# Optimization experiments

Measured on AMD Instinct MI355X. Metric: run time of the kernel, lower is better.

Reference implementation:

```python
import jax, jax.numpy as jnp
import numpy as np

B, S, H, T = 64, 512, 768, 50


def setup_inputs() -> dict:
    key = jax.random.key(0)
    k1, k2, k3, k4, k5, k6, k7 = jax.random.split(key, 7)
    full_hidden = jax.random.normal(k1, (B, S, H), dtype=jnp.float32)
    tag_ids = jax.random.randint(k2, (B, S), 0, T)
    lengths = jax.random.randint(k3, (B,), 1, S + 1)
    mask = (jnp.arange(S)[None, :] < lengths[:, None])  # valid-prefix mask, t=0 always on
    W = jax.random.normal(k4, (H, T), dtype=jnp.float32) * 0.02
    b = jnp.zeros((T,), dtype=jnp.float32)
    start_transitions = jax.random.normal(k5, (T,), dtype=jnp.float32) * 0.1
    end_transitions = jax.random.normal(k6, (T,), dtype=jnp.float32) * 0.1
    transitions = jax.random.normal(k7, (T, T), dtype=jnp.float32) * 0.1
    return {
        'full_hidden': full_hidden, 'W': W, 'b': b,
        'start_transitions': start_transitions, 'end_transitions': end_transitions,
        'transitions': transitions, 'tag_ids': tag_ids, 'mask': mask,
    }


def _crf_losses(emissions, start_transitions, end_transitions, transitions, tag_ids, mask):
    # emissions: [B,S,T]; returns per-sequence loss = log_partition - gold_score (pytorch-crf, reduction='none', negated)
    maskf = mask.astype(emissions.dtype)
    Bn = tag_ids.shape[0]
    bidx = jnp.arange(Bn)
    # ---- numerator: score of the gold tag path ----
    em_tag = jnp.take_along_axis(emissions, tag_ids[..., None], axis=2)[..., 0]  # [B,S]
    num = start_transitions[tag_ids[:, 0]] + em_tag[:, 0]
    trans_score = transitions[tag_ids[:, :-1], tag_ids[:, 1:]]  # [B,S-1]
    num = num + jnp.sum((trans_score + em_tag[:, 1:]) * maskf[:, 1:], axis=1)
    lengths = jnp.sum(mask.astype(jnp.int32), axis=1)
    last_tags = tag_ids[bidx, lengths - 1]
    num = num + end_transitions[last_tags]
    # ---- denominator: log partition via forward DP (scan over time) ----
    alpha0 = start_transitions[None, :] + emissions[:, 0]  # [B,T]

    def step(alpha, inp):
        em_t, m_t = inp  # [B,T], [B]
        nxt = jax.nn.logsumexp(alpha[:, :, None] + transitions[None, :, :] + em_t[:, None, :], axis=1)
        alpha = jnp.where(m_t[:, None], nxt, alpha)
        return alpha, None

    em_rest = jnp.swapaxes(emissions[:, 1:], 0, 1)  # [S-1,B,T]
    m_rest = jnp.swapaxes(mask[:, 1:], 0, 1)        # [S-1,B]
    alpha, _ = jax.lax.scan(step, alpha0, (em_rest, m_rest))
    den = jax.nn.logsumexp(alpha + end_transitions[None, :], axis=1)
    return den - num  # [B]


def reference(full_hidden, W, b, start_transitions, end_transitions, transitions, tag_ids, mask):
    # dropout is identity in eval mode (config dropout applied at train time only)
    emissions = jnp.einsum('bsh,ht->bst', full_hidden, W) + b  # hid2tag
    return _crf_losses(emissions, start_transitions, end_transitions, transitions, tag_ids, mask)
```

## Files before the change

kernel.cpp:

```cpp
#include <hip/hip_runtime.h>
#include <cstdint>
#include <cstddef>

#define Bn 64
#define Sn 512
#define Hn 768
#define Tn 50
#define CH 32
#define NCH 16
#define EP 52

typedef short short8 __attribute__((ext_vector_type(8)));
typedef float floatx4 __attribute__((ext_vector_type(4)));

__device__ __forceinline__ uint32_t rne_bf16(float x) {
  uint32_t u = __float_as_uint(x);
  return (u + 0x7FFFu + ((u >> 16) & 1u)) >> 16;
}
__device__ __forceinline__ uint32_t pack2(float a, float b) {
  return rne_bf16(a) | (rne_bf16(b) << 16);
}
__device__ __forceinline__ float rdlane(float v, int i) {
  return __uint_as_float(__builtin_amdgcn_readlane(__float_as_uint(v), i));
}

__global__ __launch_bounds__(256) void prep_kernel(
    const float* __restrict__ W, const float* __restrict__ trans,
    const int* __restrict__ mask, uint32_t* __restrict__ wfrag,
    int* __restrict__ lenbuf, float* __restrict__ Ee,
    float* __restrict__ EeT) {
  const int blk = blockIdx.x;
  const int tid = threadIdx.x;
  if (blk < 64) {
    if (tid < 64) {
      int s = 0;
      for (int t = tid; t < Sn; t += 64) s += mask[blk * Sn + t];
#pragma unroll
      for (int off = 1; off < 64; off <<= 1) s += __shfl_xor(s, off);
      if (tid == 0) lenbuf[blk] = s;
    }
    return;
  }
  if (blk == 88) {
    for (int gid = tid; gid < Tn * Tn; gid += 256) {
      const int r = gid / Tn, cl = gid - r * Tn;
      const float v = __expf(trans[gid]);
      Ee[r * EP + cl] = v;
      EeT[cl * EP + r] = v;
    }
    return;
  }
  const int gid = (blk - 64) * 256 + tid;
  const int f = gid >> 6;
  const int l = gid & 63;
  const int ks = f >> 2, nt = f & 3;
  const int col = nt * 16 + (l & 15);
  const int k0 = ks * 32 + (l >> 4) * 8;
  float v[8];
#pragma unroll
  for (int j = 0; j < 8; ++j)
    v[j] = (col < Tn) ? W[(size_t)(k0 + j) * Tn + col] : 0.f;
  uint4 d;
  d.x = pack2(v[0], v[1]);
  d.y = pack2(v[2], v[3]);
  d.z = pack2(v[4], v[5]);
  d.w = pack2(v[6], v[7]);
  ((uint4*)wfrag)[gid] = d;
}

#define BK 64
__global__ __launch_bounds__(256, 1) void emissions_kernel(
    const float* __restrict__ hidden, const uint32_t* __restrict__ wfrag,
    const float* __restrict__ bias, const int* __restrict__ lenbuf,
    float* __restrict__ em) {
  const int blk = blockIdx.x;
  const int bb = blk >> 3, cc = blk & 7;
  if (cc * 64 >= lenbuf[bb]) return;
  const int tid = threadIdx.x;
  const int lane = tid & 63;
  const int w = tid >> 6;
  const int g = lane >> 4;
  const int li = lane & 15;
  const int row0 = blk * 64;
  __shared__ char lds_raw[64 * 128];

  floatx4 acc[4];
#pragma unroll
  for (int nt = 0; nt < 4; ++nt) acc[nt] = (floatx4)0.f;

  const float* hbase = hidden + (size_t)row0 * Hn;
  const short8* wf = (const short8*)wfrag;

#define LOADCH(dst, ch)                                                       \
  _Pragma("unroll") for (int k = 0; k < 4; ++k) dst[k] =                      \
      *(const float4*)(hbase + (size_t)(w * 16 + 4 * k + g) * Hn + (ch)*BK +  \
                       li * 4);

#define WRITELDS(src)                                                         \
  _Pragma("unroll") for (int k = 0; k < 4; ++k) {                             \
    const int r = w * 16 + 4 * k + g;                                         \
    const uint32_t b0 = pack2(src[k].x, src[k].y);                            \
    const uint32_t b1 = pack2(src[k].z, src[k].w);                            \
    const int byteoff = r * 128 + ((li * 8) ^ ((r & 7) << 4));                \
    *(uint2*)(lds_raw + byteoff) = make_uint2(b0, b1);                        \
  }

#define COMPUTE(ch)                                                           \
  _Pragma("unroll") for (int ks = 0; ks < 2; ++ks) {                          \
    const int r = w * 16 + li;                                                \
    const int kb = ks * 64 + g * 16;                                          \
    const short8 af =                                                         \
        *(const short8*)(lds_raw + r * 128 + (kb ^ ((r & 7) << 4)));          \
    const int ksg = (ch)*2 + ks;                                              \
    _Pragma("unroll") for (int nt = 0; nt < 4; ++nt) {                        \
      const short8 bf = wf[(ksg * 4 + nt) * 64 + lane];                       \
      acc[nt] =                                                               \
          __builtin_amdgcn_mfma_f32_16x16x32_bf16(af, bf, acc[nt], 0, 0, 0);  \
    }                                                                         \
  }

  float4 pfA[4], pfB[4];
  LOADCH(pfA, 0)
  LOADCH(pfB, 1)
#pragma unroll
  for (int chp = 0; chp < Hn / BK / 2; ++chp) {
    const int ch = 2 * chp;
    WRITELDS(pfA)
    if (ch + 2 < Hn / BK) LOADCH(pfA, ch + 2)
    COMPUTE(ch)
    WRITELDS(pfB)
    if (ch + 3 < Hn / BK) LOADCH(pfB, ch + 3)
    COMPUTE(ch + 1)
  }
#undef LOADCH
#undef WRITELDS
#undef COMPUTE

#pragma unroll
  for (int nt = 0; nt < 4; ++nt) {
    const int col = nt * 16 + li;
    if (col < Tn) {
      const float bs = bias[col];
#pragma unroll
      for (int r = 0; r < 4; ++r) {
        const int row = row0 + w * 16 + g * 4 + r;
        em[(size_t)row * Tn + col] = acc[nt][r] + bs;
      }
    }
  }
}

__global__ __launch_bounds__(64, 1) void scan_kernel(
    const float* __restrict__ em, const float* __restrict__ startT,
    const float* __restrict__ trans, const float* __restrict__ Ee,
    const float* __restrict__ EeT, const int* __restrict__ tag,
    const int* __restrict__ lenbuf, float* __restrict__ fvec,
    float* __restrict__ gvec, float* __restrict__ Lf,
    float* __restrict__ numpart) {
  const int blk = blockIdx.x;
  const int b = blk >> 5;
  const int c = (blk >> 1) & (NCH - 1);
  const int dir = blk & 1;
  const int len = lenbuf[b];
  const int t0 = 1 + c * CH;
  if (t0 >= len) return;
  if (dir && c == 0) return;
  const int t1 = (t0 + CH < len) ? t0 + CH : len;
  const int L = t1 - t0;
  const int lane = threadIdx.x;
  const int jc = lane < Tn ? lane : 0;
  const bool live = lane < Tn;
  const float* emb = em + (size_t)b * Sn * Tn;

  if (!dir) {
    float npv = 0.f;
    if (lane < L) {
      const int t = t0 + lane;
      const int tp = tag[b * Sn + t - 1], tc = tag[b * Sn + t];
      npv = trans[tp * Tn + tc] + emb[(size_t)t * Tn + tc];
    }
#pragma unroll
    for (int off = 1; off < 64; off <<= 1) npv += __shfl_xor(npv, off);
    if (lane == 0) numpart[b * NCH + c] = npv;
  }

  const float* ebase = (dir ? Ee : EeT) + jc * EP;
  float e[Tn];
#pragma unroll
  for (int i = 0; i < Tn; ++i) e[i] = ebase[i];

  float Cacc = 0.f;
  float q;
  if (!dir)
    q = live ? (c == 0 ? __expf(startT[jc] + emb[jc]) : 1.f) : 0.f;
  else
    q = live ? 1.f : 0.f;

#define T_OF(k) (dir ? (t1 - 1 - (k)) : (t0 + (k)))
  float ld1 = emb[(size_t)T_OF(0) * Tn + jc];
  const float ld2 = emb[(size_t)T_OF(L > 1 ? 1 : 0) * Tn + jc];
  float ee = live ? __expf(ld1) : 0.f;
  ld1 = ld2;

  for (int k = 0; k < L; ++k) {
    const float ee_cur = ee;
    const int kn = (k + 2 < L) ? k + 2 : L - 1;
    const float ldn = emb[(size_t)T_OF(kn) * Tn + jc];
    ee = live ? __expf(ld1) : 0.f;
    ld1 = ldn;

    const float x = dir ? ee_cur * q : q;
    float s0 = 0.f, s1 = 0.f, s2 = 0.f, s3 = 0.f;
#pragma unroll
    for (int i = 0; i < 48; i += 4) {
      s0 = fmaf(rdlane(x, i + 0), e[i + 0], s0);
      s1 = fmaf(rdlane(x, i + 1), e[i + 1], s1);
      s2 = fmaf(rdlane(x, i + 2), e[i + 2], s2);
      s3 = fmaf(rdlane(x, i + 3), e[i + 3], s3);
    }
    s0 = fmaf(rdlane(x, 48), e[48], s0);
    s1 = fmaf(rdlane(x, 49), e[49], s1);
    const float s = (s0 + s1) + (s2 + s3);
    q = dir ? s : ee_cur * s;

    if ((k & 7) == 7) {
      float M = q;
#pragma unroll
      for (int off = 1; off < 64; off <<= 1) M = fmaxf(M, __shfl_xor(M, off));
      const float r = __builtin_amdgcn_rcpf(M);
      q *= r;
      Cacc -= __logf(r);
    }
  }
#undef T_OF

  float M = q;
#pragma unroll
  for (int off = 1; off < 64; off <<= 1) M = fmaxf(M, __shfl_xor(M, off));
  const float r = __builtin_amdgcn_rcpf(M);
  const float qn = live ? q * r : 0.f;
  Cacc -= __logf(r);
  if (dir) {
    gvec[((size_t)b * NCH + c) * 64 + lane] = qn;
  } else {
    fvec[((size_t)b * NCH + c) * 64 + lane] = qn;
    if (lane == 0) Lf[b * NCH + c] = Cacc;
  }
}

__global__ __launch_bounds__(64) void stitch_kernel(
    const float* __restrict__ em, const float* __restrict__ startT,
    const float* __restrict__ endT, const int* __restrict__ tag,
    const int* __restrict__ lenbuf, const float* __restrict__ fvec,
    const float* __restrict__ gvec, const float* __restrict__ Lf,
    const float* __restrict__ numpart, float* __restrict__ out) {
  const int b = blockIdx.x;
  const int lane = threadIdx.x;
  const int len = lenbuf[b];
  const int C = (len - 1 + CH - 1) / CH;
  const int jc = lane < Tn ? lane : 0;
  const bool live = lane < Tn;
  const float* emb = em + (size_t)b * Sn * Tn;

  float np = (lane < C) ? numpart[b * NCH + lane] : 0.f;
#pragma unroll
  for (int off = 1; off < 64; off <<= 1) np += __shfl_xor(np, off);
  const int tg0 = tag[b * Sn];
  const int tgl = tag[b * Sn + len - 1];
  np += startT[tg0] + emb[tg0] + endT[tgl];

  float den;
  if (C == 0) {
    float v = live ? (startT[jc] + emb[jc] + endT[jc]) : -INFINITY;
    float M = v;
#pragma unroll
    for (int off = 1; off < 64; off <<= 1) M = fmaxf(M, __shfl_xor(M, off));
    float s = __expf(v - M);
#pragma unroll
    for (int off = 1; off < 64; off <<= 1) s += __shfl_xor(s, off);
    den = M + __logf(s);
  } else {
    const float ev = live ? __expf(endT[jc]) : 0.f;
    float d = fvec[((size_t)b * NCH + C - 1) * 64 + lane] * ev;
#pragma unroll
    for (int off = 1; off < 64; off <<= 1) d += __shfl_xor(d, off);
    den = Lf[b * NCH + C - 1] + __logf(d);
    for (int c2 = 1; c2 < C; ++c2) {
      const float g = gvec[((size_t)b * NCH + c2) * 64 + lane];
      const float f = fvec[((size_t)b * NCH + c2 - 1) * 64 + lane];
      float dot = g * f;
      float gs = g;
#pragma unroll
      for (int off = 1; off < 64; off <<= 1) {
        dot += __shfl_xor(dot, off);
        gs += __shfl_xor(gs, off);
      }
      den += Lf[b * NCH + c2 - 1] + __logf(dot) - __logf(gs);
    }
  }
  if (lane == 0) out[b] = den - np;
}

extern "C" void kernel_launch(void* const* d_in, const int* in_sizes, int n_in,
                              void* d_out, int out_size, void* d_ws,
                              size_t ws_size, hipStream_t stream) {
  const float* hidden = (const float*)d_in[0];
  const float* W = (const float*)d_in[1];
  const float* bias = (const float*)d_in[2];
  const float* startT = (const float*)d_in[3];
  const float* endT = (const float*)d_in[4];
  const float* trans = (const float*)d_in[5];
  const int* tag = (const int*)d_in[6];
  const int* mask = (const int*)d_in[7];
  float* out = (float*)d_out;

  char* ws = (char*)d_ws;
  float* em = (float*)ws;
  uint32_t* wfrag = (uint32_t*)(ws + 6553600);
  int* lenbuf = (int*)(ws + 6651904);
  float* Ee = (float*)(ws + 6652160);
  float* EeT = (float*)(ws + 6662976);
  float* fvec = (float*)(ws + 6673792);
  float* gvec = (float*)(ws + 6935936);
  float* Lf = (float*)(ws + 7198080);
  float* numpart = (float*)(ws + 7202176);

  prep_kernel<<<89, 256, 0, stream>>>(W, trans, mask, wfrag, lenbuf, Ee, EeT);
  emissions_kernel<<<(Bn * Sn) / 64, 256, 0, stream>>>(hidden, wfrag, bias,
                                                       lenbuf, em);
  scan_kernel<<<Bn * NCH * 2, 64, 0, stream>>>(em, startT, trans, Ee, EeT, tag,
                                               lenbuf, fvec, gvec, Lf, numpart);
  stitch_kernel<<<Bn, 64, 0, stream>>>(em, startT, endT, tag, lenbuf, fvec,
                                       gvec, Lf, numpart, out);
}
```

Baseline: 53.16 us.

## Fuse four kernels into one cooperative persistent kernel with grid syncs

```diff
diff --git a/kernel.cpp b/kernel.cpp
--- a/kernel.cpp
+++ b/kernel.cpp
@@ -1,6 +1,9 @@
 #include <hip/hip_runtime.h>
+#include <hip/hip_cooperative_groups.h>
 #include <cstdint>
 #include <cstddef>
+
+namespace cg = cooperative_groups;
 
 #define Bn 64
 #define Sn 512
@@ -9,6 +12,7 @@
 #define CH 32
 #define NCH 16
 #define EP 52
+#define BK 64
 
 typedef short short8 __attribute__((ext_vector_type(8)));
 typedef float floatx4 __attribute__((ext_vector_type(4)));
@@ -24,281 +28,270 @@
   return __uint_as_float(__builtin_amdgcn_readlane(__float_as_uint(v), i));
 }
 
-__global__ __launch_bounds__(256) void prep_kernel(
-    const float* __restrict__ W, const float* __restrict__ trans,
-    const int* __restrict__ mask, uint32_t* __restrict__ wfrag,
-    int* __restrict__ lenbuf, float* __restrict__ Ee,
-    float* __restrict__ EeT) {
-  const int blk = blockIdx.x;
+__global__ __launch_bounds__(256, 2) void fused_kernel(
+    const float* __restrict__ hidden, const float* __restrict__ W,
+    const float* __restrict__ bias, const float* __restrict__ startT,
+    const float* __restrict__ endT, const float* __restrict__ trans,
+    const int* __restrict__ tag, const int* __restrict__ mask,
+    float* __restrict__ em, uint32_t* __restrict__ wfrag,
+    int* __restrict__ lenbuf, float* __restrict__ Ee, float* __restrict__ EeT,
+    float* __restrict__ fvec, float* __restrict__ gvec, float* __restrict__ Lf,
+    float* __restrict__ numpart, float* __restrict__ out) {
+  cg::grid_group grid = cg::this_grid();
   const int tid = threadIdx.x;
-  if (blk < 64) {
-    if (tid < 64) {
-      int s = 0;
-      for (int t = tid; t < Sn; t += 64) s += mask[blk * Sn + t];
-#pragma unroll
-      for (int off = 1; off < 64; off <<= 1) s += __shfl_xor(s, off);
-      if (tid == 0) lenbuf[blk] = s;
-    }
-    return;
-  }
-  if (blk == 88) {
-    for (int gid = tid; gid < Tn * Tn; gid += 256) {
-      const int r = gid / Tn, cl = gid - r * Tn;
-      const float v = __expf(trans[gid]);
-      Ee[r * EP + cl] = v;
-      EeT[cl * EP + r] = v;
-    }
-    return;
-  }
-  const int gid = (blk - 64) * 256 + tid;
-  const int f = gid >> 6;
-  const int l = gid & 63;
-  const int ks = f >> 2, nt = f & 3;
-  const int col = nt * 16 + (l & 15);
-  const int k0 = ks * 32 + (l >> 4) * 8;
-  float v[8];
-#pragma unroll
-  for (int j = 0; j < 8; ++j)
-    v[j] = (col < Tn) ? W[(size_t)(k0 + j) * Tn + col] : 0.f;
-  uint4 d;
-  d.x = pack2(v[0], v[1]);
-  d.y = pack2(v[2], v[3]);
-  d.z = pack2(v[4], v[5]);
-  d.w = pack2(v[6], v[7]);
-  ((uint4*)wfrag)[gid] = d;
-}
-
-#define BK 64
-__global__ __launch_bounds__(256, 1) void emissions_kernel(
-    const float* __restrict__ hidden, const uint32_t* __restrict__ wfrag,
-    const float* __restrict__ bias, const int* __restrict__ lenbuf,
-    float* __restrict__ em) {
-  const int blk = blockIdx.x;
-  const int bb = blk >> 3, cc = blk & 7;
-  if (cc * 64 >= lenbuf[bb]) return;
-  const int tid = threadIdx.x;
-  const int lane = tid & 63;
-  const int w = tid >> 6;
-  const int g = lane >> 4;
-  const int li = lane & 15;
-  const int row0 = blk * 64;
+  const int nblk = gridDim.x;
   __shared__ char lds_raw[64 * 128];
 
-  floatx4 acc[4];
-#pragma unroll
-  for (int nt = 0; nt < 4; ++nt) acc[nt] = (floatx4)0.f;
-
-  const float* hbase = hidden + (size_t)row0 * Hn;
-  const short8* wf = (const short8*)wfrag;
-
-#define LOADCH(dst, ch)                                                       \
-  _Pragma("unroll") for (int k = 0; k < 4; ++k) dst[k] =                      \
-      *(const float4*)(hbase + (size_t)(w * 16 + 4 * k + g) * Hn + (ch)*BK +  \
+  for (int task = blockIdx.x; task < 89; task += nblk) {
+    if (task < 64) {
+      if (tid < 64) {
+        int s = 0;
+        for (int t = tid; t < Sn; t += 64) s += mask[task * Sn + t];
+#pragma unroll
+        for (int off = 1; off < 64; off <<= 1) s += __shfl_xor(s, off);
+        if (tid == 0) lenbuf[task] = s;
+      }
+    } else if (task < 88) {
+      const int gid = (task - 64) * 256 + tid;
+      const int f = gid >> 6;
+      const int l = gid & 63;
+      const int ks = f >> 2, nt = f & 3;
+      const int col = nt * 16 + (l & 15);
+      const int k0 = ks * 32 + (l >> 4) * 8;
+      float v[8];
+#pragma unroll
+      for (int j = 0; j < 8; ++j)
+        v[j] = (col < Tn) ? W[(size_t)(k0 + j) * Tn + col] : 0.f;
+      uint4 d;
+      d.x = pack2(v[0], v[1]);
+      d.y = pack2(v[2], v[3]);
+      d.z = pack2(v[4], v[5]);
+      d.w = pack2(v[6], v[7]);
+      ((uint4*)wfrag)[gid] = d;
+    } else {
+      for (int gid = tid; gid < Tn * Tn; gid += 256) {
+        const int r = gid / Tn, cl = gid - r * Tn;
+        const float v = __expf(trans[gid]);
+        Ee[r * EP + cl] = v;
+        EeT[cl * EP + r] = v;
+      }
+    }
+  }
+  grid.sync();
+
+  for (int eb = blockIdx.x; eb < Bn * 8; eb += nblk) {
+    const int bb = eb >> 3, cc = eb & 7;
+    if (mask[bb * Sn + cc * 64] == 0) continue;
+    const int lane = tid & 63;
+    const int w = tid >> 6;
+    const int g = lane >> 4;
+    const int li = lane & 15;
+    const int row0 = eb * 64;
+
+    floatx4 acc[4];
+#pragma unroll
+    for (int nt = 0; nt < 4; ++nt) acc[nt] = (floatx4)0.f;
+
+    const float* hbase = hidden + (size_t)row0 * Hn;
+    const short8* wf = (const short8*)wfrag;
+
+#define LOADCH(dst, ch)                                                      \
+  _Pragma("unroll") for (int k = 0; k < 4; ++k) dst[k] =                     \
+      *(const float4*)(hbase + (size_t)(w * 16 + 4 * k + g) * Hn + (ch)*BK + \
                        li * 4);
-
-#define WRITELDS(src)                                                         \
-  _Pragma("unroll") for (int k = 0; k < 4; ++k) {                             \
-    const int r = w * 16 + 4 * k + g;                                         \
-    const uint32_t b0 = pack2(src[k].x, src[k].y);                            \
-    const uint32_t b1 = pack2(src[k].z, src[k].w);                            \
-    const int byteoff = r * 128 + ((li * 8) ^ ((r & 7) << 4));                \
-    *(uint2*)(lds_raw + byteoff) = make_uint2(b0, b1);                        \
-  }
-
-#define COMPUTE(ch)                                                           \
-  _Pragma("unroll") for (int ks = 0; ks < 2; ++ks) {                          \
-    const int r = w * 16 + li;                                                \
-    const int kb = ks * 64 + g * 16;                                          \
-    const short8 af =                                                         \
-        *(const short8*)(lds_raw + r * 128 + (kb ^ ((r & 7) << 4)));          \
-    const int ksg = (ch)*2 + ks;                                              \
-    _Pragma("unroll") for (int nt = 0; nt < 4; ++nt) {                        \
-      const short8 bf = wf[(ksg * 4 + nt) * 64 + lane];                       \
-      acc[nt] =                                                               \
-          __builtin_amdgcn_mfma_f32_16x16x32_bf16(af, bf, acc[nt], 0, 0, 0);  \
-    }                                                                         \
-  }
-
-  float4 pfA[4], pfB[4];
-  LOADCH(pfA, 0)
-  LOADCH(pfB, 1)
-#pragma unroll
-  for (int chp = 0; chp < Hn / BK / 2; ++chp) {
-    const int ch = 2 * chp;
-    WRITELDS(pfA)
-    if (ch + 2 < Hn / BK) LOADCH(pfA, ch + 2)
-    COMPUTE(ch)
-    WRITELDS(pfB)
-    if (ch + 3 < Hn / BK) LOADCH(pfB, ch + 3)
-    COMPUTE(ch + 1)
-  }
+#define WRITELDS(src)                                                        \
+  _Pragma("unroll") for (int k = 0; k < 4; ++k) {                            \
+    const int r = w * 16 + 4 * k + g;                                        \
+    const uint32_t b0 = pack2(src[k].x, src[k].y);                           \
+    const uint32_t b1 = pack2(src[k].z, src[k].w);                           \
+    const int byteoff = r * 128 + ((li * 8) ^ ((r & 7) << 4));               \
+    *(uint2*)(lds_raw + byteoff) = make_uint2(b0, b1);                       \
+  }
+#define COMPUTE(ch)                                                          \
+  _Pragma("unroll") for (int ks = 0; ks < 2; ++ks) {                         \
+    const int r = w * 16 + li;                                               \
+    const int kb = ks * 64 + g * 16;                                         \
+    const short8 af =                                                        \
+        *(const short8*)(lds_raw + r * 128 + (kb ^ ((r & 7) << 4)));         \
+    const int ksg = (ch)*2 + ks;                                             \
+    _Pragma("unroll") for (int nt = 0; nt < 4; ++nt) {                       \
+      const short8 bf = wf[(ksg * 4 + nt) * 64 + lane];                      \
+      acc[nt] =                                                              \
+          __builtin_amdgcn_mfma_f32_16x16x32_bf16(af, bf, acc[nt], 0, 0, 0); \
+    }                                                                        \
+  }
+
+    float4 pfA[4], pfB[4];
+    LOADCH(pfA, 0)
+    LOADCH(pfB, 1)
+#pragma unroll
+    for (int chp = 0; chp < Hn / BK / 2; ++chp) {
+      const int ch = 2 * chp;
+      WRITELDS(pfA)
+      if (ch + 2 < Hn / BK) LOADCH(pfA, ch + 2)
+      COMPUTE(ch)
+      WRITELDS(pfB)
+      if (ch + 3 < Hn / BK) LOADCH(pfB, ch + 3)
+      COMPUTE(ch + 1)
+    }
 #undef LOADCH
 #undef WRITELDS
 #undef COMPUTE
 
 #pragma unroll
-  for (int nt = 0; nt < 4; ++nt) {
-    const int col = nt * 16 + li;
-    if (col < Tn) {
-      const float bs = bias[col];
-#pragma unroll
-      for (int r = 0; r < 4; ++r) {
-        const int row = row0 + w * 16 + g * 4 + r;
-        em[(size_t)row * Tn + col] = acc[nt][r] + bs;
-      }
-    }
-  }
-}
-
-__global__ __launch_bounds__(64, 1) void scan_kernel(
-    const float* __restrict__ em, const float* __restrict__ startT,
-    const float* __restrict__ trans, const float* __restrict__ Ee,
-    const float* __restrict__ EeT, const int* __restrict__ tag,
-    const int* __restrict__ lenbuf, float* __restrict__ fvec,
-    float* __restrict__ gvec, float* __restrict__ Lf,
-    float* __restrict__ numpart) {
-  const int blk = blockIdx.x;
-  const int b = blk >> 5;
-  const int c = (blk >> 1) & (NCH - 1);
-  const int dir = blk & 1;
-  const int len = lenbuf[b];
-  const int t0 = 1 + c * CH;
-  if (t0 >= len) return;
-  if (dir && c == 0) return;
-  const int t1 = (t0 + CH < len) ? t0 + CH : len;
-  const int L = t1 - t0;
-  const int lane = threadIdx.x;
-  const int jc = lane < Tn ? lane : 0;
-  const bool live = lane < Tn;
-  const float* emb = em + (size_t)b * Sn * Tn;
-
-  if (!dir) {
-    float npv = 0.f;
-    if (lane < L) {
-      const int t = t0 + lane;
-      const int tp = tag[b * Sn + t - 1], tc = tag[b * Sn + t];
-      npv = trans[tp * Tn + tc] + emb[(size_t)t * Tn + tc];
-    }
-#pragma unroll
-    for (int off = 1; off < 64; off <<= 1) npv += __shfl_xor(npv, off);
-    if (lane == 0) numpart[b * NCH + c] = npv;
-  }
-
-  const float* ebase = (dir ? Ee : EeT) + jc * EP;
-  float e[Tn];
-#pragma unroll
-  for (int i = 0; i < Tn; ++i) e[i] = ebase[i];
-
-  float Cacc = 0.f;
-  float q;
-  if (!dir)
-    q = live ? (c == 0 ? __expf(startT[jc] + emb[jc]) : 1.f) : 0.f;
-  else
-    q = live ? 1.f : 0.f;
+    for (int nt = 0; nt < 4; ++nt) {
+      const int col = nt * 16 + li;
+      if (col < Tn) {
+        const float bs = bias[col];
+#pragma unroll
+        for (int r = 0; r < 4; ++r) {
+          const int row = row0 + w * 16 + g * 4 + r;
+          em[(size_t)row * Tn + col] = acc[nt][r] + bs;
+        }
+      }
+    }
+  }
+  grid.sync();
+
+  for (int tb = blockIdx.x; tb < Bn * 8; tb += nblk) {
+    const int task = tb * 4 + (tid >> 6);
+    const int lane = tid & 63;
+    const int b = task >> 5;
+    const int c = (task >> 1) & (NCH - 1);
+    const int dir = task & 1;
+    const int len = lenbuf[b];
+    const int t0 = 1 + c * CH;
+    if (t0 >= len || (dir && c == 0)) continue;
+    const int t1 = (t0 + CH < len) ? t0 + CH : len;
+    const int L = t1 - t0;
+    const int jc = lane < Tn ? lane : 0;
+    const bool live = lane < Tn;
+    const float* emb = em + (size_t)b * Sn * Tn;
+
+    if (!dir) {
+      float npv = 0.f;
+      if (lane < L) {
+        const int t = t0 + lane;
+        const int tp = tag[b * Sn + t - 1], tc = tag[b * Sn + t];
+        npv = trans[tp * Tn + tc] + emb[(size_t)t * Tn + tc];
+      }
+#pragma unroll
+      for (int off = 1; off < 64; off <<= 1) npv += __shfl_xor(npv, off);
+      if (lane == 0) numpart[b * NCH + c] = npv;
+    }
+
+    const float* ebase = (dir ? Ee : EeT) + jc * EP;
+    float e[Tn];
+#pragma unroll
+    for (int i = 0; i < Tn; ++i) e[i] = ebase[i];
+
+    float Cacc = 0.f;
+    float q;
+    if (!dir)
+      q = live ? (c == 0 ? __expf(startT[jc] + emb[jc]) : 1.f) : 0.f;
+    else
+      q = live ? 1.f : 0.f;
 
 #define T_OF(k) (dir ? (t1 - 1 - (k)) : (t0 + (k)))
-  float ld1 = emb[(size_t)T_OF(0) * Tn + jc];
-  const float ld2 = emb[(size_t)T_OF(L > 1 ? 1 : 0) * Tn + jc];
-  float ee = live ? __expf(ld1) : 0.f;
-  ld1 = ld2;
-
-  for (int k = 0; k < L; ++k) {
-    const float ee_cur = ee;
-    const int kn = (k + 2 < L) ? k + 2 : L - 1;
-    const float ldn = emb[(size_t)T_OF(kn) * Tn + jc];
-    ee = live ? __expf(ld1) : 0.f;
-    ld1 = ldn;
-
-    const float x = dir ? ee_cur * q : q;
-    float s0 = 0.f, s1 = 0.f, s2 = 0.f, s3 = 0.f;
-#pragma unroll
-    for (int i = 0; i < 48; i += 4) {
-      s0 = fmaf(rdlane(x, i + 0), e[i + 0], s0);
-      s1 = fmaf(rdlane(x, i + 1), e[i + 1], s1);
-      s2 = fmaf(rdlane(x, i + 2), e[i + 2], s2);
-      s3 = fmaf(rdlane(x, i + 3), e[i + 3], s3);
-    }
-    s0 = fmaf(rdlane(x, 48), e[48], s0);
-    s1 = fmaf(rdlane(x, 49), e[49], s1);
-    const float s = (s0 + s1) + (s2 + s3);
-    q = dir ? s : ee_cur * s;
-
-    if ((k & 7) == 7) {
-      float M = q;
+    float ld1 = emb[(size_t)T_OF(0) * Tn + jc];
+    const float ld2 = emb[(size_t)T_OF(L > 1 ? 1 : 0) * Tn + jc];
+    float ee = live ? __expf(ld1) : 0.f;
+    ld1 = ld2;
+
+    for (int k = 0; k < L; ++k) {
+      const float ee_cur = ee;
+      const int kn = (k + 2 < L) ? k + 2 : L - 1;
+      const float ldn = emb[(size_t)T_OF(kn) * Tn + jc];
+      ee = live ? __expf(ld1) : 0.f;
+      ld1 = ldn;
+
+      const float x = dir ? ee_cur * q : q;
+      float s0 = 0.f, s1 = 0.f, s2 = 0.f, s3 = 0.f;
+#pragma unroll
+      for (int i = 0; i < 48; i += 4) {
+        s0 = fmaf(rdlane(x, i + 0), e[i + 0], s0);
+        s1 = fmaf(rdlane(x, i + 1), e[i + 1], s1);
+        s2 = fmaf(rdlane(x, i + 2), e[i + 2], s2);
+        s3 = fmaf(rdlane(x, i + 3), e[i + 3], s3);
+      }
+      s0 = fmaf(rdlane(x, 48), e[48], s0);
+      s1 = fmaf(rdlane(x, 49), e[49], s1);
+      const float s = (s0 + s1) + (s2 + s3);
+      q = dir ? s : ee_cur * s;
+
+      if ((k & 7) == 7) {
+        float M = q;
+#pragma unroll
+        for (int off = 1; off < 64; off <<= 1) M = fmaxf(M, __shfl_xor(M, off));
+        const float r = __builtin_amdgcn_rcpf(M);
+        q *= r;
+        Cacc -= __logf(r);
+      }
+    }
+#undef T_OF
+
+    float M = q;
+#pragma unroll
+    for (int off = 1; off < 64; off <<= 1) M = fmaxf(M, __shfl_xor(M, off));
+    const float r = __builtin_amdgcn_rcpf(M);
+    const float qn = live ? q * r : 0.f;
+    Cacc -= __logf(r);
+    if (dir) {
+      gvec[((size_t)b * NCH + c) * 64 + lane] = qn;
+    } else {
+      fvec[((size_t)b * NCH + c) * 64 + lane] = qn;
+      if (lane == 0) Lf[b * NCH + c] = Cacc;
+    }
+  }
+  grid.sync();
+
+  for (int b = blockIdx.x; b < Bn; b += nblk) {
+    if (tid >= 64) continue;
+    const int lane = tid;
+    const int len = lenbuf[b];
+    const int C = (len - 1 + CH - 1) / CH;
+    const int jc = lane < Tn ? lane : 0;
+    const bool live = lane < Tn;
+    const float* emb = em + (size_t)b * Sn * Tn;
+
+    float np = (lane < C) ? numpart[b * NCH + lane] : 0.f;
+#pragma unroll
+    for (int off = 1; off < 64; off <<= 1) np += __shfl_xor(np, off);
+    const int tg0 = tag[b * Sn];
+    const int tgl = tag[b * Sn + len - 1];
+    np += startT[tg0] + emb[tg0] + endT[tgl];
+
+    float den;
+    if (C == 0) {
+      float v = live ? (startT[jc] + emb[jc] + endT[jc]) : -INFINITY;
+      float M = v;
 #pragma unroll
       for (int off = 1; off < 64; off <<= 1) M = fmaxf(M, __shfl_xor(M, off));
-      const float r = __builtin_amdgcn_rcpf(M);
-      q *= r;
-      Cacc -= __logf(r);
-    }
-  }
-#undef T_OF
-
-  float M = q;
-#pragma unroll
-  for (int off = 1; off < 64; off <<= 1) M = fmaxf(M, __shfl_xor(M, off));
-  const float r = __builtin_amdgcn_rcpf(M);
-  const float qn = live ? q * r : 0.f;
-  Cacc -= __logf(r);
-  if (dir) {
-    gvec[((size_t)b * NCH + c) * 64 + lane] = qn;
-  } else {
-    fvec[((size_t)b * NCH + c) * 64 + lane] = qn;
-    if (lane == 0) Lf[b * NCH + c] = Cacc;
-  }
-}
-
-__global__ __launch_bounds__(64) void stitch_kernel(
-    const float* __restrict__ em, const float* __restrict__ startT,
-    const float* __restrict__ endT, const int* __restrict__ tag,
-    const int* __restrict__ lenbuf, const float* __restrict__ fvec,
-    const float* __restrict__ gvec, const float* __restrict__ Lf,
-    const float* __restrict__ numpart, float* __restrict__ out) {
-  const int b = blockIdx.x;
-  const int lane = threadIdx.x;
-  const int len = lenbuf[b];
-  const int C = (len - 1 + CH - 1) / CH;
-  const int jc = lane < Tn ? lane : 0;
-  const bool live = lane < Tn;
-  const float* emb = em + (size_t)b * Sn * Tn;
-
-  float np = (lane < C) ? numpart[b * NCH + lane] : 0.f;
-#pragma unroll
-  for (int off = 1; off < 64; off <<= 1) np += __shfl_xor(np, off);
-  const int tg0 = tag[b * Sn];
-  const int tgl = tag[b * Sn + len - 1];
-  np += startT[tg0] + emb[tg0] + endT[tgl];
-
-  float den;
-  if (C == 0) {
-    float v = live ? (startT[jc] + emb[jc] + endT[jc]) : -INFINITY;
-    float M = v;
-#pragma unroll
-    for (int off = 1; off < 64; off <<= 1) M = fmaxf(M, __shfl_xor(M, off));
-    float s = __expf(v - M);
-#pragma unroll
-    for (int off = 1; off < 64; off <<= 1) s += __shfl_xor(s, off);
-    den = M + __logf(s);
-  } else {
-    const float ev = live ? __expf(endT[jc]) : 0.f;
-    float d = fvec[((size_t)b * NCH + C - 1) * 64 + lane] * ev;
-#pragma unroll
-    for (int off = 1; off < 64; off <<= 1) d += __shfl_xor(d, off);
-    den = Lf[b * NCH + C - 1] + __logf(d);
-    for (int c2 = 1; c2 < C; ++c2) {
-      const float g = gvec[((size_t)b * NCH + c2) * 64 + lane];
-      const float f = fvec[((size_t)b * NCH + c2 - 1) * 64 + lane];
-      float dot = g * f;
-      float gs = g;
-#pragma unroll
-      for (int off = 1; off < 64; off <<= 1) {
-        dot += __shfl_xor(dot, off);
-        gs += __shfl_xor(gs, off);
-      }
-      den += Lf[b * NCH + c2 - 1] + __logf(dot) - __logf(gs);
-    }
-  }
-  if (lane == 0) out[b] = den - np;
+      float s = __expf(v - M);
+#pragma unroll
+      for (int off = 1; off < 64; off <<= 1) s += __shfl_xor(s, off);
+      den = M + __logf(s);
+    } else {
+      const float ev = live ? __expf(endT[jc]) : 0.f;
+      float d = fvec[((size_t)b * NCH + C - 1) * 64 + lane] * ev;
+#pragma unroll
+      for (int off = 1; off < 64; off <<= 1) d += __shfl_xor(d, off);
+      den = Lf[b * NCH + C - 1] + __logf(d);
+      for (int c2 = 1; c2 < C; ++c2) {
+        const float g = gvec[((size_t)b * NCH + c2) * 64 + lane];
+        const float f = fvec[((size_t)b * NCH + c2 - 1) * 64 + lane];
+        float dot = g * f;
+        float gs = g;
+#pragma unroll
+        for (int off = 1; off < 64; off <<= 1) {
+          dot += __shfl_xor(dot, off);
+          gs += __shfl_xor(gs, off);
+        }
+        den += Lf[b * NCH + c2 - 1] + __logf(dot) - __logf(gs);
+      }
+    }
+    if (lane == 0) out[b] = den - np;
+  }
 }
 
 extern "C" void kernel_launch(void* const* d_in, const int* in_sizes, int n_in,
@@ -325,11 +318,18 @@
   float* Lf = (float*)(ws + 7198080);
   float* numpart = (float*)(ws + 7202176);
 
-  prep_kernel<<<89, 256, 0, stream>>>(W, trans, mask, wfrag, lenbuf, Ee, EeT);
-  emissions_kernel<<<(Bn * Sn) / 64, 256, 0, stream>>>(hidden, wfrag, bias,
-                                                       lenbuf, em);
-  scan_kernel<<<Bn * NCH * 2, 64, 0, stream>>>(em, startT, trans, Ee, EeT, tag,
-                                               lenbuf, fvec, gvec, Lf, numpart);
-  stitch_kernel<<<Bn, 64, 0, stream>>>(em, startT, endT, tag, lenbuf, fvec,
-                                       gvec, Lf, numpart, out);
-}
+  int nb = 0;
+  hipOccupancyMaxActiveBlocksPerMultiprocessor(&nb, fused_kernel, 256, 0);
+  if (nb < 1) nb = 1;
+  int grid = nb * 256;
+  if (grid > 512) grid = 512;
+
+  void* args[] = {(void*)&hidden, (void*)&W,      (void*)&bias,
+                  (void*)&startT, (void*)&endT,   (void*)&trans,
+                  (void*)&tag,    (void*)&mask,   (void*)&em,
+                  (void*)&wfrag,  (void*)&lenbuf, (void*)&Ee,
+                  (void*)&EeT,    (void*)&fvec,   (void*)&gvec,
+                  (void*)&Lf,     (void*)&numpart, (void*)&out};
+  hipLaunchCooperativeKernel((void*)fused_kernel, dim3(grid), dim3(256), args,
+                             0, stream);
+}
```

New measurement: 191.6 us. +260.4%, slower.
